# Optimization experiments

Hardware: AMD Instinct MI355X
Metric: run time of the kernel (lower is better)

The kernel has to match this reference:

```python
import jax, jax.numpy as jnp
import numpy as np

HEADS = 8
DIM_HEAD = 32


def setup_inputs() -> dict:
    key = jax.random.key(0)
    ks = jax.random.split(key, 10)
    B, N, D = 64, 256, 256            # B = b_true * tie_dim = 1 * 64
    INNER = HEADS * DIM_HEAD          # 256
    x = jax.random.normal(ks[0], (B, N, D), dtype=jnp.float32)
    mask = jax.random.randint(ks[1], (B, N), 0, 2).astype(bool)
    attn_bias = jax.random.normal(ks[2], (1, HEADS, N, N), dtype=jnp.float32)
    # Note: original init zeros to_out/gating weights; we use random params
    # (scaled) so the baseline output is non-trivial for correctness testing.
    s = 0.05
    Wq = jax.random.normal(ks[3], (D, INNER), dtype=jnp.float32) * s
    Wkv = jax.random.normal(ks[4], (D, 2 * INNER), dtype=jnp.float32) * s
    Wg = jax.random.normal(ks[5], (D, INNER), dtype=jnp.float32) * s
    bg = jax.random.normal(ks[6], (INNER,), dtype=jnp.float32) * s
    Wo = jax.random.normal(ks[7], (INNER, D), dtype=jnp.float32) * s
    bo = jax.random.normal(ks[8], (D,), dtype=jnp.float32) * s
    return {"x": x, "mask": mask, "attn_bias": attn_bias, "Wq": Wq,
            "Wkv": Wkv, "Wg": Wg, "bg": bg, "Wo": Wo, "bo": bo,
            "tie_dim": 64}


def reference(x, mask, attn_bias, Wq, Wkv, Wg, bg, Wo, bo, tie_dim):
    B, N, D = x.shape
    h, dh = HEADS, DIM_HEAD
    scale = dh ** -0.5

    # projections (self-attention: context = x)
    q = (x @ Wq).reshape(B, N, h, dh).transpose(0, 2, 1, 3) * scale  # b h n d
    k, v = jnp.split(x @ Wkv, 2, axis=-1)
    k = k.reshape(B, N, h, dh).transpose(0, 2, 1, 3)                 # b h n d
    v = v.reshape(B, N, h, dh).transpose(0, 2, 1, 3)                 # b h n d

    # tie_dim: average q over the r (MSA row) dim, keep per-row k
    r = tie_dim
    b = B // r
    q_tied = q.reshape(b, r, h, N, dh).mean(axis=1)                  # b h i d
    k_r = k.reshape(b, r, h, N, dh)                                  # b r h j d
    dots = jnp.einsum('bhid,brhjd->brhij', q_tied, k_r)
    dots = dots.reshape(B, h, N, N)                                  # (b r) h i j

    dots = dots + attn_bias

    # mask: pairwise row/col mask (context_mask == mask for self-attn)
    pair_mask = mask[:, None, :, None] & mask[:, None, None, :]      # B 1 i j
    mask_value = -jnp.finfo(dots.dtype).max
    dots = jnp.where(pair_mask, dots, mask_value)

    attn = jax.nn.softmax(dots, axis=-1)
    out = jnp.einsum('bhij,bhjd->bhid', attn, v)
    out = out.transpose(0, 2, 1, 3).reshape(B, N, h * dh)            # b n (h d)

    gates = jax.nn.sigmoid(x @ Wg + bg)
    out = out * gates
    return out @ Wo + bo
```

## Files before the change

kernel.cpp:

```cpp
#include <hip/hip_runtime.h>
#include <math.h>

typedef unsigned short ushort_t;
typedef unsigned int uint_t;
typedef __attribute__((ext_vector_type(8))) short short8v;
typedef __attribute__((ext_vector_type(4))) float f32x4;

#define NEG_MAX (-3.402823466e+38f)

#define OFF_KH    0
#define OFF_VP    4194304
#define OFF_GATES 6291456
#define OFF_XHI   8388608
#define OFF_ATTHI OFF_XHI
#define OFF_BTHI  12582912
#define OFF_BTLO  12713984
#define OFF_QTH   12845056
#define OFF_BIASP 12976128
#define OFF_MASK  13500416

__device__ __forceinline__ ushort_t f2bf(float x) {
    uint_t u = __float_as_uint(x);
    u = (u + 0x7fffu + ((u >> 16) & 1u)) >> 16;
    return (ushort_t)u;
}
__device__ __forceinline__ float bf2f(ushort_t u) {
    return __uint_as_float(((uint_t)u) << 16);
}
__device__ __forceinline__ void gl2lds16(const void* g, void* l) {
    typedef const __attribute__((address_space(1))) uint32_t* gptr_t;
    typedef __attribute__((address_space(3))) uint32_t* lptr_t;
    __builtin_amdgcn_global_load_lds((gptr_t)(uintptr_t)g,
                                     (lptr_t)(uintptr_t)l, 16, 0, 0);
}

__global__ __launch_bounds__(256) void prep_kernel(
    const float* __restrict__ x, const unsigned char* __restrict__ mraw,
    const float* __restrict__ bias, const float* __restrict__ Wkv,
    const float* __restrict__ Wg, const float* __restrict__ Wo,
    const float* __restrict__ Wq,
    ushort_t* __restrict__ xhi,
    int* __restrict__ maskc,
    ushort_t* __restrict__ bthi, ushort_t* __restrict__ btlo,
    float* __restrict__ biasP, ushort_t* __restrict__ qPh) {
    __shared__ int cnt[256];
    __shared__ float xrow[256];
    const int bid = blockIdx.x, t = threadIdx.x;
    if (bid < 4096) {
        int idx = bid * 256 + t;
        float4 v = ((const float4*)x)[idx];
        ushort4 h;
        h.x = f2bf(v.x);
        h.y = f2bf(v.y);
        h.z = f2bf(v.z);
        h.w = f2bf(v.w);
        ((ushort4*)xhi)[idx] = h;
    } else if (bid < 4112) {
        int c = 0;
        for (int i = t; i < 4096; i += 256)
            if ((i & 3) != 0 && mraw[i] != 0) c++;
        cnt[t] = c;
        __syncthreads();
        for (int s = 128; s > 0; s >>= 1) {
            if (t < s) cnt[t] += cnt[t + s];
            __syncthreads();
        }
        int isBool = cnt[0] > 16;
        int base = (bid - 4096) * 1024;
        if (isBool) {
            for (int i = t; i < 1024; i += 256)
                maskc[base + i] = mraw[base + i] ? 1 : 0;
        } else {
            const int* mi = (const int*)mraw;
            for (int i = t; i < 1024; i += 256)
                maskc[base + i] = mi[base + i] ? 1 : 0;
        }
    } else if (bid < 5136) {
        int idx = (bid - 4112) * 256 + t;
        int n = idx >> 8, k = idx & 255;
        float v;
        if (n < 512)      v = Wkv[(size_t)k * 512 + n];
        else if (n < 768) v = Wg[(size_t)k * 256 + (n - 512)];
        else              v = Wo[(size_t)k * 256 + (n - 768)];
        ushort_t h = f2bf(v);
        bthi[idx] = h;
        btlo[idx] = f2bf(v - bf2f(h));
    } else if (bid < 5648) {
        int idx = (bid - 5136) * 256 + t;
        int lane = idx & 63, g2 = idx >> 6;
        int mf = g2 & 3, nf = (g2 >> 2) & 1, jt = (g2 >> 3) & 3;
        int iq = (g2 >> 5) & 7, h = g2 >> 8;
        int lr = lane & 15, lg = lane >> 4;
        float4 v = *(const float4*)(bias +
            (size_t)(h * 256 + iq * 32 + nf * 16 + lr) * 256 +
            jt * 64 + mf * 16 + lg * 4);
        *(float4*)(biasP + (size_t)idx * 4) = v;
    } else {
        int i = bid - 5648;
        float s0 = 0.f, s1 = 0.f, s2 = 0.f, s3 = 0.f;
#pragma unroll
        for (int b8 = 0; b8 < 64; b8 += 4) {
            s0 += x[(size_t)(b8 * 256 + i) * 256 + t];
            s1 += x[(size_t)((b8 + 1) * 256 + i) * 256 + t];
            s2 += x[(size_t)((b8 + 2) * 256 + i) * 256 + t];
            s3 += x[(size_t)((b8 + 3) * 256 + i) * 256 + t];
        }
        xrow[t] = ((s0 + s1) + (s2 + s3)) * (1.0f / 64.0f);
        __syncthreads();
        float s = 0.f;
        for (int k = 0; k < 256; k++)
            s = fmaf(xrow[k], Wq[(size_t)k * 256 + t], s);
        s *= 0.17677669529663687f;
        int h = t >> 5, d = t & 31, lg = d >> 3, e = d & 7;
        int g = i >> 4, lr = i & 15;
        int a = (((h * 16 + g) * 4 + lg) * 16 + lr) * 8 + e;
        qPh[a] = f2bf(s);
    }
}

template <int EPI, int MT, int NT, int TERMS>
__global__ __launch_bounds__(256) void mfma_gemm(
    const ushort_t* __restrict__ Ahi, const ushort_t* __restrict__ Alo,
    const ushort_t* __restrict__ Bthi, const ushort_t* __restrict__ Btlo,
    const float* __restrict__ bias, float* __restrict__ C,
    ushort_t* __restrict__ kh, ushort_t* __restrict__ vP,
    ushort_t* __restrict__ gatesP, int gridn) {
    constexpr int BM = MT * 32, BN = NT * 32;
    constexpr int ASZ = BM * 32 * 2;
    constexpr int BSZ = BN * 32 * 2;
    constexpr bool HAS_AL = (TERMS == 2 || TERMS == 3);
    constexpr bool HAS_BL = (TERMS == 3 || TERMS == 4);
    constexpr int AL_OFF = 2 * ASZ;
    constexpr int BH_OFF = AL_OFF + (HAS_AL ? 2 * ASZ : 0);
    constexpr int BL_OFF = BH_OFF + 2 * BSZ;
    constexpr int SMEM_BYTES = BL_OFF + (HAS_BL ? 2 * BSZ : 0);
    __shared__ __align__(16) char smem[SMEM_BYTES];
    char* aH = smem;
    char* aL = smem + AL_OFF;
    char* bH = smem + BH_OFF;
    char* bL = smem + BL_OFF;

    const int t = threadIdx.x;
    const int nwg = gridDim.x, cpx = nwg >> 3;
    const int bid = blockIdx.x;
    const int sid = (bid & 7) * cpx + (bid >> 3);
    const int m0 = (sid / gridn) * BM;
    const int n0 = (sid % gridn) * BN;
    const int wid = t >> 6, lane = t & 63;
    const int wr = wid >> 1, wc = wid & 1;
    const int lr = lane & 15, lg = lane >> 4;

    auto STAGE = [&](int d, int ks) {
        const int k0 = ks * 32;
#pragma unroll
        for (int it = 0; it < BM / 64; ++it) {
            int c = t + it * 256;
            int row = c >> 2, sub = c & 3;
            size_t ga = (size_t)(m0 + row) * 256 + k0 + sub * 8;
            gl2lds16(Ahi + ga, aH + d * ASZ + c * 16);
            if constexpr (HAS_AL)
                gl2lds16(Alo + ga, aL + d * ASZ + c * 16);
        }
#pragma unroll
        for (int it = 0; it < BN / 64; ++it) {
            int c = t + it * 256;
            int row = c >> 2, sub = c & 3;
            size_t gb = (size_t)(n0 + row) * 256 + k0 + sub * 8;
            gl2lds16(Bthi + gb, bH + d * BSZ + c * 16);
            if constexpr (HAS_BL)
                gl2lds16(Btlo + gb, bL + d * BSZ + c * 16);
        }
    };

    f32x4 acc[MT][NT] = {};

    STAGE(0, 0);
    asm volatile("s_waitcnt vmcnt(0)" ::: "memory");
    __syncthreads();

    int cur = 0;
    for (int ks = 0; ks < 8; ++ks) {
        if (ks < 7) STAGE(cur ^ 1, ks + 1);

        const ushort_t* Ap = (const ushort_t*)(aH + cur * ASZ);
        const ushort_t* ALp = (const ushort_t*)(aL + cur * ASZ);
        const ushort_t* Bp = (const ushort_t*)(bH + cur * BSZ);
        const ushort_t* BLp = (const ushort_t*)(bL + cur * BSZ);

        short8v ah[MT], al[MT], bh[NT], bl[NT];
#pragma unroll
        for (int m = 0; m < MT; m++) {
            int off = (wr * (MT * 16) + m * 16 + lr) * 32 + lg * 8;
            ah[m] = *(const short8v*)&Ap[off];
            if constexpr (HAS_AL) al[m] = *(const short8v*)&ALp[off];
        }
#pragma unroll
        for (int n = 0; n < NT; n++) {
            int off = (wc * (NT * 16) + n * 16 + lr) * 32 + lg * 8;
            bh[n] = *(const short8v*)&Bp[off];
            if constexpr (HAS_BL) bl[n] = *(const short8v*)&BLp[off];
        }
#pragma unroll
        for (int m = 0; m < MT; m++)
#pragma unroll
            for (int n = 0; n < NT; n++) {
                acc[m][n] = __builtin_amdgcn_mfma_f32_16x16x32_bf16(
                    ah[m], bh[n], acc[m][n], 0, 0, 0);
                if constexpr (HAS_AL)
                    acc[m][n] = __builtin_amdgcn_mfma_f32_16x16x32_bf16(
                        al[m], bh[n], acc[m][n], 0, 0, 0);
                if constexpr (HAS_BL)
                    acc[m][n] = __builtin_amdgcn_mfma_f32_16x16x32_bf16(
                        ah[m], bl[n], acc[m][n], 0, 0, 0);
            }

        if (ks < 7) {
            asm volatile("s_waitcnt vmcnt(0)" ::: "memory");
            __syncthreads();
        }
        cur ^= 1;
    }

#pragma unroll
    for (int m = 0; m < MT; m++)
#pragma unroll
        for (int n = 0; n < NT; n++) {
            int gr0 = m0 + wr * (MT * 16) + m * 16 + lg * 4;
            int gc = n0 + wc * (NT * 16) + n * 16 + lr;
            if (EPI == 0) {
                if (gc < 256) {
                    int hh_ = gc >> 5, dk = gc & 31;
                    int lgk = dk >> 3, ek = dk & 7;
#pragma unroll
                    for (int r = 0; r < 4; r++) {
                        int gr = gr0 + r;
                        int bb = gr >> 8, j = gr & 255;
                        int jt = j >> 6, mfk = (j >> 4) & 3, lrk = j & 15;
                        size_t a =
                            (((((size_t)(bb * 8 + hh_) * 4 + jt) * 4 + mfk) * 4
                              + lgk) * 16 + lrk) * 8 + ek;
                        kh[a] = f2bf(acc[m][n][r]);
                    }
                } else if (gc < 512) {
                    int cc = gc - 256;
                    int hh_ = cc >> 5, dv = cc & 31;
                    int mfv = dv >> 4, lrv = dv & 15;
                    int gr = gr0;
                    int bb = gr >> 8, j = gr & 255;
                    int jt = j >> 6, hbv = (j >> 5) & 1;
                    int lgv = (j >> 3) & 3, ev = j & 7;
                    size_t a =
                        ((((((size_t)(bb * 8 + hh_) * 4 + jt) * 2 + hbv) * 2
                           + mfv) * 4 + lgv) * 16 + lrv) * 8 + ev;
                    ushort4 hv;
                    hv.x = f2bf(acc[m][n][0]);
                    hv.y = f2bf(acc[m][n][1]);
                    hv.z = f2bf(acc[m][n][2]);
                    hv.w = f2bf(acc[m][n][3]);
                    *(ushort4*)(vP + a) = hv;
                } else {
                    int c = gc - 512;
                    int hh_ = c >> 5, d = c & 31;
                    int mdv = d >> 4, lga = (d >> 2) & 3, ev = d & 3;
#pragma unroll
                    for (int r = 0; r < 4; r++) {
                        int gr = gr0 + r;
                        int bb = gr >> 8, i = gr & 255;
                        int i16 = i >> 4, lra = i & 15;
                        size_t a =
                            ((((size_t)(bb * 8 + hh_) * 16 + i16) * 2 + mdv)
                             * 64 + lga * 16 + lra) * 4 + ev;
                        float v = acc[m][n][r];
                        float g = 1.f / (1.f + __expf(-(v + bias[gc - 512])));
                        gatesP[a] = f2bf(g);
                    }
                }
            } else {
#pragma unroll
                for (int r = 0; r < 4; r++)
                    C[(size_t)(gr0 + r) * 256 + gc] = acc[m][n][r] + bias[gc];
            }
        }
}

__global__ __launch_bounds__(256) void attn_mfma_kernel(
    const ushort_t* __restrict__ qPh, const ushort_t* __restrict__ kh,
    const ushort_t* __restrict__ vP, const ushort_t* __restrict__ gatesP,
    const float* __restrict__ biasP, const int* __restrict__ mask,
    ushort_t* __restrict__ atthi) {
    __shared__ __align__(16) ushort_t Pb[4][16 * 88];
    const int bid = blockIdx.x;
    const int sid = ((bid & 7) << 8) | (bid >> 3);
    const int b = sid >> 5;
    const int h = (sid >> 2) & 7;
    const int qq = sid & 3;
    const int t = threadIdx.x;
    const int w = t >> 6, lane = t & 63;
    const int lr = lane & 15, lg = lane >> 4;
    const int i0 = qq * 64 + w * 16;
    const int i16 = qq * 4 + w;
    ushort_t* pbh = Pb[w];

    short8v qf;
    {
        size_t off = ((((size_t)h * 16 + i16) * 4 + lg) * 16 + lr) * 8;
        qf = *(const short8v*)(qPh + off);
    }
    const int mi = mask[b * 256 + i0 + lr];

    const float* bbase = biasP +
        (size_t)(h * 256 + (i16 >> 1) * 32 + (i16 & 1) * 4) * 256 +
        (size_t)lane * 4;

    float m_run = NEG_MAX, l_run = 0.f;
    f32x4 acc_o[2] = {};

    short8v kf[2][4];
    float4 bf[2][4];
#pragma unroll
    for (int mf = 0; mf < 4; mf++) {
        size_t off = ((((size_t)(b * 8 + h) * 4 + 0) * 4 + mf) * 4 + lg);
        kf[0][mf] = *(const short8v*)(kh + (off * 16 + lr) * 8);
        bf[0][mf] = *(const float4*)(bbase + (size_t)mf * 256);
    }

#pragma unroll
    for (int jt = 0; jt < 4; ++jt) {
        const int cur = jt & 1, nxt = cur ^ 1;
        if (jt < 3) {
#pragma unroll
            for (int mf = 0; mf < 4; mf++) {
                size_t off = ((((size_t)(b * 8 + h) * 4 + (jt + 1)) * 4 + mf)
                              * 4 + lg);
                kf[nxt][mf] = *(const short8v*)(kh + (off * 16 + lr) * 8);
                bf[nxt][mf] = *(const float4*)(bbase +
                                               (size_t)((jt + 1) * 8 + mf) * 256);
            }
        }
        short8v vf[2][2];
#pragma unroll
        for (int hb = 0; hb < 2; hb++)
#pragma unroll
            for (int mv = 0; mv < 2; mv++) {
                size_t off = ((((((size_t)(b * 8 + h) * 4 + jt) * 2 + hb) * 2
                               + mv) * 4 + lg) * 16 + lr) * 8;
                vf[hb][mv] = *(const short8v*)(vP + off);
            }
        int4 mj[4];
#pragma unroll
        for (int mf = 0; mf < 4; mf++)
            mj[mf] = *(const int4*)(mask + b * 256 + jt * 64 + mf * 16 + lg * 4);

        f32x4 s[4];
        __builtin_amdgcn_s_setprio(1);
#pragma unroll
        for (int mf = 0; mf < 4; mf++) {
            f32x4 a = {};
            s[mf] = __builtin_amdgcn_mfma_f32_16x16x32_bf16(
                kf[cur][mf], qf, a, 0, 0, 0);
        }
        __builtin_amdgcn_s_setprio(0);
#pragma unroll
        for (int mf = 0; mf < 4; mf++) {
            float4 bv = bf[cur][mf];
            s[mf][0] = (mi && mj[mf].x) ? s[mf][0] + bv.x : NEG_MAX;
            s[mf][1] = (mi && mj[mf].y) ? s[mf][1] + bv.y : NEG_MAX;
            s[mf][2] = (mi && mj[mf].z) ? s[mf][2] + bv.z : NEG_MAX;
            s[mf][3] = (mi && mj[mf].w) ? s[mf][3] + bv.w : NEG_MAX;
        }

        float tm = s[0][0];
#pragma unroll
        for (int mf = 0; mf < 4; mf++)
#pragma unroll
            for (int r = 0; r < 4; r++) tm = fmaxf(tm, s[mf][r]);
        tm = fmaxf(tm, __shfl_xor(tm, 16));
        tm = fmaxf(tm, __shfl_xor(tm, 32));
        float mnew = fmaxf(m_run, tm);
        float corr = __expf(m_run - mnew);
        m_run = mnew;
#pragma unroll
        for (int md = 0; md < 2; md++)
#pragma unroll
            for (int r = 0; r < 4; r++) acc_o[md][r] *= corr;
        float ls = 0.f;
#pragma unroll
        for (int mf = 0; mf < 4; mf++)
#pragma unroll
            for (int r = 0; r < 4; r++) {
                float wv = __expf(s[mf][r] - mnew);
                s[mf][r] = wv;
                ls += wv;
            }
        ls += __shfl_xor(ls, 16);
        ls += __shfl_xor(ls, 32);
        l_run = l_run * corr + ls;

#pragma unroll
        for (int mf = 0; mf < 4; mf++) {
            uint2 hv;
            hv.x = (uint_t)f2bf(s[mf][0]) | ((uint_t)f2bf(s[mf][1]) << 16);
            hv.y = (uint_t)f2bf(s[mf][2]) | ((uint_t)f2bf(s[mf][3]) << 16);
            *(uint2*)(pbh + lr * 88 + mf * 16 + lg * 4) = hv;
        }
        asm volatile("s_waitcnt lgkmcnt(0)" ::: "memory");
        __builtin_amdgcn_sched_barrier(0);
        short8v ph0 = *(const short8v*)(pbh + lr * 88 + lg * 8);
        short8v ph1 = *(const short8v*)(pbh + lr * 88 + 32 + lg * 8);
        __builtin_amdgcn_s_setprio(1);
        acc_o[0] = __builtin_amdgcn_mfma_f32_16x16x32_bf16(
            vf[0][0], ph0, acc_o[0], 0, 0, 0);
        acc_o[1] = __builtin_amdgcn_mfma_f32_16x16x32_bf16(
            vf[0][1], ph0, acc_o[1], 0, 0, 0);
        acc_o[0] = __builtin_amdgcn_mfma_f32_16x16x32_bf16(
            vf[1][0], ph1, acc_o[0], 0, 0, 0);
        acc_o[1] = __builtin_amdgcn_mfma_f32_16x16x32_bf16(
            vf[1][1], ph1, acc_o[1], 0, 0, 0);
        __builtin_amdgcn_s_setprio(0);
    }

    float invl = 1.0f / l_run;
#pragma unroll
    for (int md = 0; md < 2; md++) {
        size_t ga = ((((size_t)(b * 8 + h) * 16 + i16) * 2 + md) * 64 + lane) * 4;
        uint2 gv = *(const uint2*)(gatesP + ga);
        float g0 = bf2f((ushort_t)(gv.x & 0xffff));
        float g1 = bf2f((ushort_t)(gv.x >> 16));
        float g2 = bf2f((ushort_t)(gv.y & 0xffff));
        float g3 = bf2f((ushort_t)(gv.y >> 16));
        int i = i0 + lr;
        int d0 = md * 16 + lg * 4;
        size_t base = ((size_t)(b * 256 + i)) * 256 + h * 32 + d0;
        ushort4 hh;
        hh.x = f2bf(acc_o[md][0] * invl * g0);
        hh.y = f2bf(acc_o[md][1] * invl * g1);
        hh.z = f2bf(acc_o[md][2] * invl * g2);
        hh.w = f2bf(acc_o[md][3] * invl * g3);
        *(ushort4*)(atthi + base) = hh;
    }
}

extern "C" void kernel_launch(void* const* d_in, const int* in_sizes, int n_in,
                              void* d_out, int out_size, void* d_ws, size_t ws_size,
                              hipStream_t stream) {
    const float* x    = (const float*)d_in[0];
    const unsigned char* mraw = (const unsigned char*)d_in[1];
    const float* bias = (const float*)d_in[2];
    const float* Wq   = (const float*)d_in[3];
    const float* Wkv  = (const float*)d_in[4];
    const float* Wg   = (const float*)d_in[5];
    const float* bg   = (const float*)d_in[6];
    const float* Wo   = (const float*)d_in[7];
    const float* bo   = (const float*)d_in[8];

    float* ws = (float*)d_ws;
    ushort_t* kh     = (ushort_t*)(ws + OFF_KH);
    ushort_t* vP     = (ushort_t*)(ws + OFF_VP);
    ushort_t* gatesP = (ushort_t*)(ws + OFF_GATES);
    ushort_t* xhi    = (ushort_t*)(ws + OFF_XHI);
    ushort_t* atthi  = (ushort_t*)(ws + OFF_ATTHI);
    ushort_t* bthi   = (ushort_t*)(ws + OFF_BTHI);
    ushort_t* btlo   = (ushort_t*)(ws + OFF_BTLO);
    ushort_t* qPh    = (ushort_t*)(ws + OFF_QTH);
    float*    biasP  = ws + OFF_BIASP;
    int*      maskc  = (int*)(ws + OFF_MASK);

    hipLaunchKernelGGL(prep_kernel, dim3(5904), dim3(256), 0, stream,
                       x, mraw, bias, Wkv, Wg, Wo, Wq,
                       xhi, maskc, bthi, btlo, biasP, qPh);
    hipLaunchKernelGGL((mfma_gemm<0, 4, 4, 1>), dim3(768), dim3(256), 0, stream,
                       xhi, xhi, bthi, btlo, bg, (float*)nullptr,
                       kh, vP, gatesP, 6);
    hipLaunchKernelGGL(attn_mfma_kernel, dim3(2048), dim3(256), 0, stream,
                       qPh, kh, vP, gatesP, biasP, maskc, atthi);
    hipLaunchKernelGGL((mfma_gemm<1, 2, 4, 4>), dim3(512), dim3(256), 0, stream,
                       atthi, atthi, bthi + 768 * 256, btlo + 768 * 256, bo,
                       (float*)d_out, nullptr, nullptr, nullptr, 2);
}
```

Baseline: 81.99 us.

## Bit-pack mask, prefetch V tiles and gates, retile output GEMM

```diff
diff --git a/kernel.cpp b/kernel.cpp
--- a/kernel.cpp
+++ b/kernel.cpp
@@ -40,7 +40,7 @@
     const float* __restrict__ Wg, const float* __restrict__ Wo,
     const float* __restrict__ Wq,
     ushort_t* __restrict__ xhi,
-    int* __restrict__ maskc,
+    uint_t* __restrict__ maskb,
     ushort_t* __restrict__ bthi, ushort_t* __restrict__ btlo,
     float* __restrict__ biasP, ushort_t* __restrict__ qPh) {
     __shared__ int cnt[256];
@@ -55,7 +55,7 @@
         h.z = f2bf(v.z);
         h.w = f2bf(v.w);
         ((ushort4*)xhi)[idx] = h;
-    } else if (bid < 4112) {
+    } else if (bid < 4097) {
         int c = 0;
         for (int i = t; i < 4096; i += 256)
             if ((i & 3) != 0 && mraw[i] != 0) c++;
@@ -66,17 +66,23 @@
             __syncthreads();
         }
         int isBool = cnt[0] > 16;
-        int base = (bid - 4096) * 1024;
-        if (isBool) {
-            for (int i = t; i < 1024; i += 256)
-                maskc[base + i] = mraw[base + i] ? 1 : 0;
-        } else {
-            const int* mi = (const int*)mraw;
-            for (int i = t; i < 1024; i += 256)
-                maskc[base + i] = mi[base + i] ? 1 : 0;
-        }
-    } else if (bid < 5136) {
-        int idx = (bid - 4112) * 256 + t;
+        const int* mi32 = (const int*)mraw;
+#pragma unroll
+        for (int wq = 0; wq < 2; wq++) {
+            int widx = t * 2 + wq;
+            int j0 = widx * 32;
+            uint_t wordv = 0;
+            if (isBool) {
+                for (int k = 0; k < 32; k++)
+                    wordv |= (mraw[j0 + k] ? 1u : 0u) << k;
+            } else {
+                for (int k = 0; k < 32; k++)
+                    wordv |= (mi32[j0 + k] ? 1u : 0u) << k;
+            }
+            maskb[widx] = wordv;
+        }
+    } else if (bid < 5121) {
+        int idx = (bid - 4097) * 256 + t;
         int n = idx >> 8, k = idx & 255;
         float v;
         if (n < 512)      v = Wkv[(size_t)k * 512 + n];
@@ -85,8 +91,8 @@
         ushort_t h = f2bf(v);
         bthi[idx] = h;
         btlo[idx] = f2bf(v - bf2f(h));
-    } else if (bid < 5648) {
-        int idx = (bid - 5136) * 256 + t;
+    } else if (bid < 5633) {
+        int idx = (bid - 5121) * 256 + t;
         int lane = idx & 63, g2 = idx >> 6;
         int mf = g2 & 3, nf = (g2 >> 2) & 1, jt = (g2 >> 3) & 3;
         int iq = (g2 >> 5) & 7, h = g2 >> 8;
@@ -96,7 +102,7 @@
             jt * 64 + mf * 16 + lg * 4);
         *(float4*)(biasP + (size_t)idx * 4) = v;
     } else {
-        int i = bid - 5648;
+        int i = bid - 5633;
         float s0 = 0.f, s1 = 0.f, s2 = 0.f, s3 = 0.f;
 #pragma unroll
         for (int b8 = 0; b8 < 64; b8 += 4) {
@@ -286,7 +292,7 @@
 __global__ __launch_bounds__(256) void attn_mfma_kernel(
     const ushort_t* __restrict__ qPh, const ushort_t* __restrict__ kh,
     const ushort_t* __restrict__ vP, const ushort_t* __restrict__ gatesP,
-    const float* __restrict__ biasP, const int* __restrict__ mask,
+    const float* __restrict__ biasP, const uint_t* __restrict__ maskb,
     ushort_t* __restrict__ atthi) {
     __shared__ __align__(16) ushort_t Pb[4][16 * 88];
     const int bid = blockIdx.x;
@@ -301,12 +307,22 @@
     const int i16 = qq * 4 + w;
     ushort_t* pbh = Pb[w];
 
+    uint_t mw[8];
+#pragma unroll
+    for (int k = 0; k < 8; k++) mw[k] = maskb[b * 8 + k];
+    const uint_t mi = (mw[i0 >> 5] >> ((i0 & 31) + lr)) & 1u;
+
     short8v qf;
     {
         size_t off = ((((size_t)h * 16 + i16) * 4 + lg) * 16 + lr) * 8;
         qf = *(const short8v*)(qPh + off);
     }
-    const int mi = mask[b * 256 + i0 + lr];
+    uint2 gva, gvb;
+    {
+        size_t ga = ((((size_t)(b * 8 + h) * 16 + i16) * 2 + 0) * 64 + lane) * 4;
+        gva = *(const uint2*)(gatesP + ga);
+        gvb = *(const uint2*)(gatesP + ga + 256);
+    }
 
     const float* bbase = biasP +
         (size_t)(h * 256 + (i16 >> 1) * 32 + (i16 & 1) * 4) * 256 +
@@ -317,12 +333,21 @@
 
     short8v kf[2][4];
     float4 bf[2][4];
+    short8v vf[2][2][2];
 #pragma unroll
     for (int mf = 0; mf < 4; mf++) {
         size_t off = ((((size_t)(b * 8 + h) * 4 + 0) * 4 + mf) * 4 + lg);
         kf[0][mf] = *(const short8v*)(kh + (off * 16 + lr) * 8);
         bf[0][mf] = *(const float4*)(bbase + (size_t)mf * 256);
     }
+#pragma unroll
+    for (int hb = 0; hb < 2; hb++)
+#pragma unroll
+        for (int mv = 0; mv < 2; mv++) {
+            size_t off = ((((((size_t)(b * 8 + h) * 4 + 0) * 2 + hb) * 2
+                           + mv) * 4 + lg) * 16 + lr) * 8;
+            vf[0][hb][mv] = *(const short8v*)(vP + off);
+        }
 
 #pragma unroll
     for (int jt = 0; jt < 4; ++jt) {
@@ -336,20 +361,15 @@
                 bf[nxt][mf] = *(const float4*)(bbase +
                                                (size_t)((jt + 1) * 8 + mf) * 256);
             }
-        }
-        short8v vf[2][2];
-#pragma unroll
-        for (int hb = 0; hb < 2; hb++)
-#pragma unroll
-            for (int mv = 0; mv < 2; mv++) {
-                size_t off = ((((((size_t)(b * 8 + h) * 4 + jt) * 2 + hb) * 2
-                               + mv) * 4 + lg) * 16 + lr) * 8;
-                vf[hb][mv] = *(const short8v*)(vP + off);
-            }
-        int4 mj[4];
-#pragma unroll
-        for (int mf = 0; mf < 4; mf++)
-            mj[mf] = *(const int4*)(mask + b * 256 + jt * 64 + mf * 16 + lg * 4);
+#pragma unroll
+            for (int hb = 0; hb < 2; hb++)
+#pragma unroll
+                for (int mv = 0; mv < 2; mv++) {
+                    size_t off = ((((((size_t)(b * 8 + h) * 4 + (jt + 1)) * 2
+                                    + hb) * 2 + mv) * 4 + lg) * 16 + lr) * 8;
+                    vf[nxt][hb][mv] = *(const short8v*)(vP + off);
+                }
+        }
 
         f32x4 s[4];
         __builtin_amdgcn_s_setprio(1);
@@ -360,13 +380,15 @@
                 kf[cur][mf], qf, a, 0, 0, 0);
         }
         __builtin_amdgcn_s_setprio(0);
+
 #pragma unroll
         for (int mf = 0; mf < 4; mf++) {
             float4 bv = bf[cur][mf];
-            s[mf][0] = (mi && mj[mf].x) ? s[mf][0] + bv.x : NEG_MAX;
-            s[mf][1] = (mi && mj[mf].y) ? s[mf][1] + bv.y : NEG_MAX;
-            s[mf][2] = (mi && mj[mf].z) ? s[mf][2] + bv.z : NEG_MAX;
-            s[mf][3] = (mi && mj[mf].w) ? s[mf][3] + bv.w : NEG_MAX;
+            uint_t bits = (mw[jt * 2 + (mf >> 1)] >> (((mf & 1) << 4) + (lg << 2)));
+            s[mf][0] = ((mi & bits) & 1u)        ? s[mf][0] + bv.x : NEG_MAX;
+            s[mf][1] = ((mi & (bits >> 1)) & 1u) ? s[mf][1] + bv.y : NEG_MAX;
+            s[mf][2] = ((mi & (bits >> 2)) & 1u) ? s[mf][2] + bv.z : NEG_MAX;
+            s[mf][3] = ((mi & (bits >> 3)) & 1u) ? s[mf][3] + bv.w : NEG_MAX;
         }
 
         float tm = s[0][0];
@@ -409,21 +431,20 @@
         short8v ph1 = *(const short8v*)(pbh + lr * 88 + 32 + lg * 8);
         __builtin_amdgcn_s_setprio(1);
         acc_o[0] = __builtin_amdgcn_mfma_f32_16x16x32_bf16(
-            vf[0][0], ph0, acc_o[0], 0, 0, 0);
+            vf[cur][0][0], ph0, acc_o[0], 0, 0, 0);
         acc_o[1] = __builtin_amdgcn_mfma_f32_16x16x32_bf16(
-            vf[0][1], ph0, acc_o[1], 0, 0, 0);
+            vf[cur][0][1], ph0, acc_o[1], 0, 0, 0);
         acc_o[0] = __builtin_amdgcn_mfma_f32_16x16x32_bf16(
-            vf[1][0], ph1, acc_o[0], 0, 0, 0);
+            vf[cur][1][0], ph1, acc_o[0], 0, 0, 0);
         acc_o[1] = __builtin_amdgcn_mfma_f32_16x16x32_bf16(
-            vf[1][1], ph1, acc_o[1], 0, 0, 0);
+            vf[cur][1][1], ph1, acc_o[1], 0, 0, 0);
         __builtin_amdgcn_s_setprio(0);
     }
 
     float invl = 1.0f / l_run;
 #pragma unroll
     for (int md = 0; md < 2; md++) {
-        size_t ga = ((((size_t)(b * 8 + h) * 16 + i16) * 2 + md) * 64 + lane) * 4;
-        uint2 gv = *(const uint2*)(gatesP + ga);
+        uint2 gv = (md == 0) ? gva : gvb;
         float g0 = bf2f((ushort_t)(gv.x & 0xffff));
         float g1 = bf2f((ushort_t)(gv.x >> 16));
         float g2 = bf2f((ushort_t)(gv.y & 0xffff));
@@ -463,17 +484,17 @@
     ushort_t* btlo   = (ushort_t*)(ws + OFF_BTLO);
     ushort_t* qPh    = (ushort_t*)(ws + OFF_QTH);
     float*    biasP  = ws + OFF_BIASP;
-    int*      maskc  = (int*)(ws + OFF_MASK);
-
-    hipLaunchKernelGGL(prep_kernel, dim3(5904), dim3(256), 0, stream,
+    uint_t*   maskb  = (uint_t*)(ws + OFF_MASK);
+
+    hipLaunchKernelGGL(prep_kernel, dim3(5889), dim3(256), 0, stream,
                        x, mraw, bias, Wkv, Wg, Wo, Wq,
-                       xhi, maskc, bthi, btlo, biasP, qPh);
+                       xhi, maskb, bthi, btlo, biasP, qPh);
     hipLaunchKernelGGL((mfma_gemm<0, 4, 4, 1>), dim3(768), dim3(256), 0, stream,
                        xhi, xhi, bthi, btlo, bg, (float*)nullptr,
                        kh, vP, gatesP, 6);
     hipLaunchKernelGGL(attn_mfma_kernel, dim3(2048), dim3(256), 0, stream,
-                       qPh, kh, vP, gatesP, biasP, maskc, atthi);
-    hipLaunchKernelGGL((mfma_gemm<1, 2, 4, 4>), dim3(512), dim3(256), 0, stream,
+                       qPh, kh, vP, gatesP, biasP, maskb, atthi);
+    hipLaunchKernelGGL((mfma_gemm<1, 2, 2, 4>), dim3(1024), dim3(256), 0, stream,
                        atthi, atthi, bthi + 768 * 256, btlo + 768 * 256, bo,
-                       (float*)d_out, nullptr, nullptr, nullptr, 2);
-}
+                       (float*)d_out, nullptr, nullptr, nullptr, 4);
+}
```

New measurement: 82.34 us. No clear change (+0.4%).
